# Kernel tuning notes

Measured on AMD Instinct MI355X. Metric: run time of the kernel, lower is better.

Reference implementation:

```python
import jax, jax.numpy as jnp
import numpy as np

B, L, F, H, K = 2048, 256, 64, 32, 2  # batch, seq len, features, g_hidden, LocalHilDim

def _dense_init(key, fan_in, fan_out):
    return (jax.random.normal(key, (fan_in, fan_out), jnp.float32) / np.sqrt(fan_in).astype(np.float32))

def setup_inputs() -> dict:
    key = jax.random.key(0)
    ks = jax.random.split(key, 12)
    s = jax.random.randint(ks[0], (B, L), 0, K)
    g = jax.random.normal(ks[1], (B,), jnp.float32)
    return dict(
        s=s, g=g,
        W_emb=_dense_init(ks[2], K, F), b_emb=jnp.zeros((F,), jnp.float32),
        W_g1=_dense_init(ks[3], 1, H), b_g1=jnp.zeros((H,), jnp.float32),
        W_g2=_dense_init(ks[4], H, F), b_g2=jnp.zeros((F,), jnp.float32),
        W_gh=_dense_init(ks[5], 1, F), b_gh=jnp.zeros((F,), jnp.float32),
        W_gc=_dense_init(ks[6], 1, F), b_gc=jnp.zeros((F,), jnp.float32),
        Wi=_dense_init(ks[7], F, 4 * F),  # fused input->gates (flax LSTMCell ii/if/ig/io, no bias)
        Wh=_dense_init(ks[8], F, 4 * F),  # fused hidden->gates (hi/hf/hg/ho)
        b_lstm=jnp.zeros((4 * F,), jnp.float32),  # fused gate biases
        W_amp=_dense_init(ks[9], F, K), b_amp=jnp.zeros((K,), jnp.float32),
    )

def reference(s, g, W_emb, b_emb, W_g1, b_g1, W_g2, b_g2, W_gh, b_gh, W_gc, b_gc, Wi, Wh, b_lstm, W_amp, b_amp):
    logProbFactor = 1.0
    g_in = g[:, None]                                            # [B,1]
    g_vec = jnp.tanh(g_in @ W_g1 + b_g1) @ W_g2 + b_g2          # g_mlp -> [B,F]
    h0 = g_in @ W_gh + b_gh                                      # init_carry h [B,F]
    c0 = g_in @ W_gc + b_gc                                      # init_carry c [B,F]
    s_pad = jnp.pad(s, ((0, 0), (1, 0)))                         # [B,L+1], leading 0 token
    seqy = jax.nn.one_hot(s_pad, K, dtype=jnp.float32)           # [B,L+1,K]
    emb = seqy @ W_emb + b_emb + g_vec[:, None, :]               # [B,L+1,F]
    # precompute input-side gate projections once: [B,L+1,4F]
    x_proj = emb @ Wi + b_lstm

    def step(carry, xt):                                         # xt: [B,4F]
        h, c = carry
        z = xt + h @ Wh
        zi, zf, zg, zo = jnp.split(z, 4, axis=-1)
        c = jax.nn.sigmoid(zf) * c + jax.nn.sigmoid(zi) * jnp.tanh(zg)
        h = jax.nn.sigmoid(zo) * jnp.tanh(c)
        return (h, c), h

    _, ys = jax.lax.scan(step, (h0, c0), jnp.swapaxes(x_proj, 0, 1))  # ys: [L+1,B,F]
    y = jnp.swapaxes(ys, 0, 1)                                   # [B,L+1,F]
    logits = y[:, :-1, :] @ W_amp + b_amp                        # [B,L,K]
    logp = jax.nn.log_softmax(logits) * logProbFactor
    token_logp = jnp.take_along_axis(logp, s[..., None], axis=-1)[..., 0]  # [B,L]
    return token_logp.sum(axis=-1)                               # [B]
```

## Files before the change

kernel.cpp:

```cpp
#include <hip/hip_runtime.h>


typedef __attribute__((ext_vector_type(8))) short bf16x8;
typedef __attribute__((ext_vector_type(4))) float f32x4;

#define L2E 1.44269504088896340736f
#define LN2 0.69314718055994530942f

__device__ __forceinline__ short f2bf(float x) {
    unsigned u = __builtin_bit_cast(unsigned, x);
    unsigned r = (u + 0x7FFFu + ((u >> 16) & 1u)) >> 16;
    return (short)r;
}

__global__ __launch_bounds__(256, 1) void lstm_kernel(
    const int* __restrict__ s, const float* __restrict__ g,
    const float* __restrict__ W_emb, const float* __restrict__ b_emb,
    const float* __restrict__ W_g1, const float* __restrict__ b_g1,
    const float* __restrict__ W_g2, const float* __restrict__ b_g2,
    const float* __restrict__ W_gh, const float* __restrict__ b_gh,
    const float* __restrict__ W_gc, const float* __restrict__ b_gc,
    const float* __restrict__ Wi, const float* __restrict__ Wh,
    const float* __restrict__ b_lstm, const float* __restrict__ W_amp,
    const float* __restrict__ b_amp, float* __restrict__ out)
{
    __shared__ float Bx[35 * 256];
    __shared__ unsigned char sp_l[260];
    __shared__ __align__(16) short Hb[2][640];
    __shared__ float red[4][8];

    const int tid = threadIdx.x;
    const int w   = tid >> 6;
    const int l   = tid & 63;
    const int n2  = l & 15;
    const int q   = l >> 4;
    const int wgb = blockIdx.x * 8;

    {
        const int n = tid;
        const float sc = (n >= 128 && n < 192) ? (-2.0f * L2E) : (-L2E);
        float acc[35];
        #pragma unroll
        for (int i = 0; i < 35; ++i) acc[i] = 0.f;
        for (int f = 0; f < 64; ++f) {
            float wi = Wi[f * 256 + n] * sc;
            #pragma unroll
            for (int k = 0; k < 32; ++k) acc[k] += W_g2[k * 64 + f] * wi;
            acc[32] += W_emb[f] * wi;
            acc[33] += W_emb[64 + f] * wi;
            acc[34] += (b_emb[f] + b_g2[f]) * wi;
        }
        acc[34] += b_lstm[n] * sc;
        #pragma unroll
        for (int i = 0; i < 35; ++i) Bx[i * 256 + n] = acc[i];
    }
    {
        unsigned v = 0;
        #pragma unroll
        for (int b = 0; b < 8; ++b)
            v |= (unsigned)(s[(wgb + b) * 256 + tid] & 1) << b;
        sp_l[tid + 1] = (unsigned char)v;
        if (tid == 0) sp_l[0] = 0;
    }
    __syncthreads();

    bf16x8 Bf[4][2];
    float  Dsel[4];
    f32x4  C0b[4];
    {
        bf16x8 B2f[4];
        float c0add[4];
        #pragma unroll
        for (int gi = 0; gi < 4; ++gi) {
            const int n = gi * 64 + w * 16 + n2;
            const float scg = (gi == 2) ? (-2.0f * L2E) : (-L2E);
            #pragma unroll
            for (int kf = 0; kf < 2; ++kf)
                #pragma unroll
                for (int j = 0; j < 8; ++j)
                    Bf[gi][kf][j] = f2bf(Wh[(kf * 32 + q * 8 + j) * 256 + n] * scg);
            #pragma unroll
            for (int j = 0; j < 8; ++j)
                B2f[gi][j] = f2bf(Bx[(q * 8 + j) * 256 + n]);
            c0add[gi] = Bx[32 * 256 + n] + Bx[34 * 256 + n];
            Dsel[gi]  = Bx[33 * 256 + n] - Bx[32 * 256 + n];
        }
        const float g_a = g[wgb + ((l & 15) >> 1)];
        bf16x8 Atv;
        #pragma unroll
        for (int j = 0; j < 8; ++j) {
            int k = q * 8 + j;
            Atv[j] = f2bf(tanhf(g_a * W_g1[k] + b_g1[k]));
        }
        const f32x4 zero4 = {0.f, 0.f, 0.f, 0.f};
        #pragma unroll
        for (int gi = 0; gi < 4; ++gi) {
            f32x4 c = __builtin_amdgcn_mfma_f32_16x16x32_bf16(Atv, B2f[gi], zero4, 0, 0, 0);
            float cvA = c[0] + c0add[gi];
            float cvB = c[2] + c0add[gi];
            C0b[gi][0] = cvA; C0b[gi][1] = cvA; C0b[gi][2] = cvB; C0b[gi][3] = cvB;
        }
    }
    bf16x8 BLd0, BLd1;
    f32x4 CL0;
    {
        #pragma unroll
        for (int j = 0; j < 8; ++j) {
            int k = q * 8 + j;
            BLd0[j] = (n2 == 0) ? f2bf(W_amp[k * 2 + 1] - W_amp[k * 2]) : (short)0;
            BLd1[j] = (n2 == 0) ? f2bf(W_amp[(k + 32) * 2 + 1] - W_amp[(k + 32) * 2]) : (short)0;
        }
        float bd = (n2 == 0) ? (b_amp[1] - b_amp[0]) : 0.f;
        CL0[0] = bd; CL0[1] = bd; CL0[2] = bd; CL0[3] = bd;
    }

    const int fcol   = w * 16 + n2;
    const int bA     = q * 2;
    const int bB     = bA + 1;
    const int haddrA = bA * 80 + fcol;
    const int haddrB = haddrA + 80;
    float csA, csB;
    {
        float gA = g[wgb + bA], gB = g[wgb + bB];
        csA = (-2.0f * L2E) * (gA * W_gc[fcol] + b_gc[fcol]);
        csB = (-2.0f * L2E) * (gB * W_gc[fcol] + b_gc[fcol]);
        Hb[0][haddrA] = f2bf(gA * W_gh[fcol] + b_gh[fcol]);
        Hb[0][haddrB] = f2bf(gB * W_gh[fcol] + b_gh[fcol]);
    }
    __syncthreads();

    const int ra = ((l & 15) >> 1) * 80 + q * 8;
    float slpA = 0.f, slpB = 0.f;
    unsigned spt = 0;

    auto step = [&](int t, int rb, int slot, bool doGate) {
        bf16x8 a0 = *(const bf16x8*)&Hb[rb][ra];
        bf16x8 a1 = *(const bf16x8*)&Hb[rb][ra + 32];
        unsigned spt_n = sp_l[t + 1];
        const unsigned bitA = (spt >> bA) & 1u;
        const unsigned bitB = (spt >> bB) & 1u;
        const float fA = (float)bitA, fB = (float)bitB;

        f32x4 acc[4];
        #pragma unroll
        for (int gi = 0; gi < 4; ++gi) {
            f32x4 a = __builtin_amdgcn_mfma_f32_16x16x32_bf16(a1, Bf[gi][1], C0b[gi], 0, 0, 0);
            acc[gi] = __builtin_amdgcn_mfma_f32_16x16x32_bf16(a0, Bf[gi][0], a, 0, 0, 0);
        }

        const bool rr = (w == slot) && (t >= 1);
        float dLA = 0.f, dLB = 0.f;
        if (rr) {
            f32x4 aL = __builtin_amdgcn_mfma_f32_16x16x32_bf16(a1, BLd1, CL0, 0, 0, 0);
            aL = __builtin_amdgcn_mfma_f32_16x16x32_bf16(a0, BLd0, aL, 0, 0, 0);
            dLA = aL[0]; dLB = aL[2];
        }

        if (doGate) {
            float yiA = __builtin_fmaf(fA, Dsel[0], acc[0][0]);
            float yiB = __builtin_fmaf(fB, Dsel[0], acc[0][2]);
            float yfA = __builtin_fmaf(fA, Dsel[1], acc[1][0]);
            float yfB = __builtin_fmaf(fB, Dsel[1], acc[1][2]);
            float ygA = __builtin_fmaf(fA, Dsel[2], acc[2][0]);
            float ygB = __builtin_fmaf(fB, Dsel[2], acc[2][2]);
            float yoA = __builtin_fmaf(fA, Dsel[3], acc[3][0]);
            float yoB = __builtin_fmaf(fB, Dsel[3], acc[3][2]);
            float siA = __builtin_amdgcn_rcpf(1.0f + __builtin_amdgcn_exp2f(yiA));
            float siB = __builtin_amdgcn_rcpf(1.0f + __builtin_amdgcn_exp2f(yiB));
            float sfA = __builtin_amdgcn_rcpf(1.0f + __builtin_amdgcn_exp2f(yfA));
            float sfB = __builtin_amdgcn_rcpf(1.0f + __builtin_amdgcn_exp2f(yfB));
            float rgA = __builtin_amdgcn_rcpf(1.0f + __builtin_amdgcn_exp2f(ygA));
            float rgB = __builtin_amdgcn_rcpf(1.0f + __builtin_amdgcn_exp2f(ygB));
            float soA = __builtin_amdgcn_rcpf(1.0f + __builtin_amdgcn_exp2f(yoA));
            float soB = __builtin_amdgcn_rcpf(1.0f + __builtin_amdgcn_exp2f(yoB));
            float tgsA = __builtin_fmaf(-4.0f * L2E, rgA, 2.0f * L2E);
            float tgsB = __builtin_fmaf(-4.0f * L2E, rgB, 2.0f * L2E);
            csA = __builtin_fmaf(sfA, csA, siA * tgsA);
            csB = __builtin_fmaf(sfB, csB, siB * tgsB);
            float r5A = __builtin_amdgcn_rcpf(1.0f + __builtin_amdgcn_exp2f(csA));
            float r5B = __builtin_amdgcn_rcpf(1.0f + __builtin_amdgcn_exp2f(csB));
            float thA = __builtin_fmaf(2.0f, r5A, -1.0f);
            float thB = __builtin_fmaf(2.0f, r5B, -1.0f);
            float hA  = soA * thA;
            float hB  = soB * thB;
            unsigned hv;
            asm("v_cvt_pk_bf16_f32 %0, %1, %2" : "=v"(hv) : "v"(hA), "v"(hB));
            Hb[1 - rb][haddrA] = (short)hv;
            Hb[1 - rb][haddrB] = (short)(hv >> 16);
        }
        const unsigned bAc = bitA, bBc = bitB;
        spt = spt_n;
        __syncthreads();

        if (rr) {
            float xA = bAc ? -dLA : dLA;
            float xB = bBc ? -dLB : dLB;
            float eA = __builtin_amdgcn_exp2f(L2E * xA);
            float eB = __builtin_amdgcn_exp2f(L2E * xB);
            slpA -= LN2 * __builtin_amdgcn_logf(1.0f + eA);
            slpB -= LN2 * __builtin_amdgcn_logf(1.0f + eB);
        }
    };

    for (int t0 = 0; t0 < 256; t0 += 4) {
        step(t0 + 0, 0, 0, true);
        step(t0 + 1, 1, 1, true);
        step(t0 + 2, 0, 2, true);
        step(t0 + 3, 1, 3, true);
    }
    step(256, 0, 0, false);

    if (n2 == 0) { red[w][bA] = slpA; red[w][bB] = slpB; }
    __syncthreads();
    if (tid < 8)
        out[wgb + tid] = red[0][tid] + red[1][tid] + red[2][tid] + red[3][tid];
}

extern "C" void kernel_launch(void* const* d_in, const int* in_sizes, int n_in,
                              void* d_out, int out_size, void* d_ws, size_t ws_size,
                              hipStream_t stream) {
    (void)in_sizes; (void)n_in; (void)out_size; (void)d_ws; (void)ws_size;
    const int*   s      = (const int*)d_in[0];
    const float* g      = (const float*)d_in[1];
    const float* W_emb  = (const float*)d_in[2];
    const float* b_emb  = (const float*)d_in[3];
    const float* W_g1   = (const float*)d_in[4];
    const float* b_g1   = (const float*)d_in[5];
    const float* W_g2   = (const float*)d_in[6];
    const float* b_g2   = (const float*)d_in[7];
    const float* W_gh   = (const float*)d_in[8];
    const float* b_gh   = (const float*)d_in[9];
    const float* W_gc   = (const float*)d_in[10];
    const float* b_gc   = (const float*)d_in[11];
    const float* Wi     = (const float*)d_in[12];
    const float* Wh     = (const float*)d_in[13];
    const float* b_lstm = (const float*)d_in[14];
    const float* W_amp  = (const float*)d_in[15];
    const float* b_amp  = (const float*)d_in[16];
    float* out = (float*)d_out;

    lstm_kernel<<<256, 256, 0, stream>>>(s, g, W_emb, b_emb, W_g1, b_g1, W_g2, b_g2,
                                         W_gh, b_gh, W_gc, b_gc, Wi, Wh, b_lstm,
                                         W_amp, b_amp, out);
}
```

Measured before the change: 195.5 us.

## Defer log-softmax to epilogue and fold selector bias into MFMA accumulator init

Moves the per-step softplus/log computation for the output logits out of the serial recurrence: each step now only stores the logit difference to shared memory, and a parallel epilogue computes log-sigmoid terms and reduces them across all threads. The token-dependent input contribution (Dsel) is now added to the MFMA accumulator init before the matrix multiply, which removes eight FMAs from the gate critical path after the MFMAs. It also drops the min-blocks launch bound and merges the token-bit packing into the weight-precompute block. This costs 8 KB of extra shared memory and an additional reduction phase at the end.

```diff
diff --git a/kernel.cpp b/kernel.cpp
--- a/kernel.cpp
+++ b/kernel.cpp
@@ -13,7 +13,7 @@
     return (short)r;
 }
 
-__global__ __launch_bounds__(256, 1) void lstm_kernel(
+__global__ __launch_bounds__(256) void lstm_kernel(
     const int* __restrict__ s, const float* __restrict__ g,
     const float* __restrict__ W_emb, const float* __restrict__ b_emb,
     const float* __restrict__ W_g1, const float* __restrict__ b_g1,
@@ -27,7 +27,8 @@
     __shared__ float Bx[35 * 256];
     __shared__ unsigned char sp_l[260];
     __shared__ __align__(16) short Hb[2][640];
-    __shared__ float red[4][8];
+    __shared__ __align__(16) float dLb[256 * 8];
+    __shared__ float red2[8][32];
 
     const int tid = threadIdx.x;
     const int w   = tid >> 6;
@@ -53,14 +54,12 @@
         acc[34] += b_lstm[n] * sc;
         #pragma unroll
         for (int i = 0; i < 35; ++i) Bx[i * 256 + n] = acc[i];
-    }
-    {
         unsigned v = 0;
         #pragma unroll
         for (int b = 0; b < 8; ++b)
-            v |= (unsigned)(s[(wgb + b) * 256 + tid] & 1) << b;
-        sp_l[tid + 1] = (unsigned char)v;
-        if (tid == 0) sp_l[0] = 0;
+            v |= (unsigned)(s[(wgb + b) * 256 + n] & 1) << b;
+        sp_l[n + 1] = (unsigned char)v;
+        if (n == 0) sp_l[0] = 0;
     }
     __syncthreads();
 
@@ -102,7 +101,6 @@
         }
     }
     bf16x8 BLd0, BLd1;
-    f32x4 CL0;
     {
         #pragma unroll
         for (int j = 0; j < 8; ++j) {
@@ -110,8 +108,6 @@
             BLd0[j] = (n2 == 0) ? f2bf(W_amp[k * 2 + 1] - W_amp[k * 2]) : (short)0;
             BLd1[j] = (n2 == 0) ? f2bf(W_amp[(k + 32) * 2 + 1] - W_amp[(k + 32) * 2]) : (short)0;
         }
-        float bd = (n2 == 0) ? (b_amp[1] - b_amp[0]) : 0.f;
-        CL0[0] = bd; CL0[1] = bd; CL0[2] = bd; CL0[3] = bd;
     }
 
     const int fcol   = w * 16 + n2;
@@ -130,41 +126,41 @@
     __syncthreads();
 
     const int ra = ((l & 15) >> 1) * 80 + q * 8;
-    float slpA = 0.f, slpB = 0.f;
     unsigned spt = 0;
 
     auto step = [&](int t, int rb, int slot, bool doGate) {
         bf16x8 a0 = *(const bf16x8*)&Hb[rb][ra];
         bf16x8 a1 = *(const bf16x8*)&Hb[rb][ra + 32];
         unsigned spt_n = sp_l[t + 1];
-        const unsigned bitA = (spt >> bA) & 1u;
-        const unsigned bitB = (spt >> bB) & 1u;
-        const float fA = (float)bitA, fB = (float)bitB;
+        const float fA = (float)((spt >> bA) & 1u);
+        const float fB = (float)((spt >> bB) & 1u);
 
         f32x4 acc[4];
         #pragma unroll
         for (int gi = 0; gi < 4; ++gi) {
-            f32x4 a = __builtin_amdgcn_mfma_f32_16x16x32_bf16(a1, Bf[gi][1], C0b[gi], 0, 0, 0);
+            f32x4 ci = C0b[gi];
+            ci[0] = __builtin_fmaf(fA, Dsel[gi], ci[0]);
+            ci[2] = __builtin_fmaf(fB, Dsel[gi], ci[2]);
+            f32x4 a = __builtin_amdgcn_mfma_f32_16x16x32_bf16(a1, Bf[gi][1], ci, 0, 0, 0);
             acc[gi] = __builtin_amdgcn_mfma_f32_16x16x32_bf16(a0, Bf[gi][0], a, 0, 0, 0);
         }
 
         const bool rr = (w == slot) && (t >= 1);
-        float dLA = 0.f, dLB = 0.f;
         if (rr) {
-            f32x4 aL = __builtin_amdgcn_mfma_f32_16x16x32_bf16(a1, BLd1, CL0, 0, 0, 0);
+            const f32x4 z4 = {0.f, 0.f, 0.f, 0.f};
+            f32x4 aL = __builtin_amdgcn_mfma_f32_16x16x32_bf16(a1, BLd1, z4, 0, 0, 0);
             aL = __builtin_amdgcn_mfma_f32_16x16x32_bf16(a0, BLd0, aL, 0, 0, 0);
-            dLA = aL[0]; dLB = aL[2];
+            if (n2 == 0) {
+                float2 d2; d2.x = aL[0]; d2.y = aL[2];
+                *(float2*)&dLb[(t - 1) * 8 + 2 * q] = d2;
+            }
         }
 
         if (doGate) {
-            float yiA = __builtin_fmaf(fA, Dsel[0], acc[0][0]);
-            float yiB = __builtin_fmaf(fB, Dsel[0], acc[0][2]);
-            float yfA = __builtin_fmaf(fA, Dsel[1], acc[1][0]);
-            float yfB = __builtin_fmaf(fB, Dsel[1], acc[1][2]);
-            float ygA = __builtin_fmaf(fA, Dsel[2], acc[2][0]);
-            float ygB = __builtin_fmaf(fB, Dsel[2], acc[2][2]);
-            float yoA = __builtin_fmaf(fA, Dsel[3], acc[3][0]);
-            float yoB = __builtin_fmaf(fB, Dsel[3], acc[3][2]);
+            float yiA = acc[0][0], yiB = acc[0][2];
+            float yfA = acc[1][0], yfB = acc[1][2];
+            float ygA = acc[2][0], ygB = acc[2][2];
+            float yoA = acc[3][0], yoB = acc[3][2];
             float siA = __builtin_amdgcn_rcpf(1.0f + __builtin_amdgcn_exp2f(yiA));
             float siB = __builtin_amdgcn_rcpf(1.0f + __builtin_amdgcn_exp2f(yiB));
             float sfA = __builtin_amdgcn_rcpf(1.0f + __builtin_amdgcn_exp2f(yfA));
@@ -188,18 +184,8 @@
             Hb[1 - rb][haddrA] = (short)hv;
             Hb[1 - rb][haddrB] = (short)(hv >> 16);
         }
-        const unsigned bAc = bitA, bBc = bitB;
         spt = spt_n;
         __syncthreads();
-
-        if (rr) {
-            float xA = bAc ? -dLA : dLA;
-            float xB = bBc ? -dLB : dLB;
-            float eA = __builtin_amdgcn_exp2f(L2E * xA);
-            float eB = __builtin_amdgcn_exp2f(L2E * xB);
-            slpA -= LN2 * __builtin_amdgcn_logf(1.0f + eA);
-            slpB -= LN2 * __builtin_amdgcn_logf(1.0f + eB);
-        }
     };
 
     for (int t0 = 0; t0 < 256; t0 += 4) {
@@ -210,10 +196,40 @@
     }
     step(256, 0, 0, false);
 
-    if (n2 == 0) { red[w][bA] = slpA; red[w][bB] = slpB; }
-    __syncthreads();
-    if (tid < 8)
-        out[wgb + tid] = red[0][tid] + red[1][tid] + red[2][tid] + red[3][tid];
+    {
+        const float bd = b_amp[1] - b_amp[0];
+        unsigned bits = (unsigned)sp_l[tid + 1];
+        f32x4 v0 = *(const f32x4*)&dLb[tid * 8];
+        f32x4 v1 = *(const f32x4*)&dLb[tid * 8 + 4];
+        f32x4 s0, s1;
+        #pragma unroll
+        for (int r = 0; r < 4; ++r) {
+            float d0 = v0[r] + bd;
+            float x0 = ((bits >> r) & 1u) ? -d0 : d0;
+            s0[r] = __builtin_amdgcn_logf(1.0f + __builtin_amdgcn_exp2f(L2E * x0));
+            float d1 = v1[r] + bd;
+            float x1 = ((bits >> (r + 4)) & 1u) ? -d1 : d1;
+            s1[r] = __builtin_amdgcn_logf(1.0f + __builtin_amdgcn_exp2f(L2E * x1));
+        }
+        *(f32x4*)&dLb[tid * 8]     = s0;
+        *(f32x4*)&dLb[tid * 8 + 4] = s1;
+        __syncthreads();
+        {
+            int b = tid >> 5, j = tid & 31;
+            float sum = 0.f;
+            #pragma unroll
+            for (int k = 0; k < 8; ++k)
+                sum += dLb[(j * 8 + k) * 8 + b];
+            red2[b][j] = sum;
+        }
+        __syncthreads();
+        if (tid < 8) {
+            float sum = 0.f;
+            #pragma unroll
+            for (int j2 = 0; j2 < 32; ++j2) sum += red2[tid][j2];
+            out[wgb + tid] = -LN2 * sum;
+        }
+    }
 }
 
 extern "C" void kernel_launch(void* const* d_in, const int* in_sizes, int n_in,
```

Result: slower. 203.4 us (+4.0%).
